# Kernel optimization log

Measured on AMD Instinct MI355X. Metric: run time of the kernel, lower is better.

The kernel has to match this reference:

```python
import jax, jax.numpy as jnp
import numpy as np
import math

IN_C = 1024
OUT_C = 1024
HEADS = 16
GROUPS = 4

def grouped_linear(src, weight, bias):
    # src: [..., in_c]; weight: [g, in_c//g, out_c//g]; bias: [out_c]
    g, icg, ocg = weight.shape
    lead = src.shape[:-1]
    s = src.reshape(*lead, g, icg)
    out = jnp.einsum('...gi,gio->...go', s, weight)
    out = out.reshape(*lead, g * ocg)
    return out + bias

def restricted_softmax(src, margin=0.0):
    src_max = jnp.maximum(jnp.max(src, axis=-1, keepdims=True), 0.0)
    out = jnp.exp(src - src_max)
    return out / (jnp.sum(out, axis=-1, keepdims=True) + jnp.exp(margin - src_max))

def setup_inputs() -> dict:
    key = jax.random.key(0)
    ks = jax.random.split(key, 9)
    B, S = 2, 2048
    icg, ocg = IN_C // GROUPS, OUT_C // GROUPS
    scale = 1.0 / math.sqrt(icg)
    return {
        'query': jax.random.normal(ks[0], (B, S, IN_C), jnp.float32),
        'key': jax.random.normal(ks[1], (B, S, IN_C), jnp.float32),
        'value': jax.random.normal(ks[2], (B, S, IN_C), jnp.float32),
        'wq': jax.random.uniform(ks[3], (GROUPS, icg, ocg), jnp.float32, -scale, scale),
        'wk': jax.random.uniform(ks[4], (GROUPS, icg, ocg), jnp.float32, -scale, scale),
        'wv': jax.random.uniform(ks[5], (GROUPS, icg, ocg), jnp.float32, -scale, scale),
        'bq': jax.random.uniform(ks[6], (OUT_C,), jnp.float32, -scale, scale),
        'bk': jax.random.uniform(ks[7], (OUT_C,), jnp.float32, -scale, scale),
        'bv': jax.random.uniform(ks[8], (OUT_C,), jnp.float32, -scale, scale),
    }

def reference(query, key, value, wq, wk, wv, bq, bk, bv):
    q = grouped_linear(query, wq, bq)   # [B,S,OUT_C]
    k = grouped_linear(key, wk, bk)
    v = grouped_linear(value, wv, bv)
    B, Sq, _ = q.shape
    Sk = k.shape[-2]
    d = OUT_C // HEADS
    q = q.reshape(B, Sq, HEADS, d).transpose(0, 2, 1, 3)  # [B,H,Sq,d]
    k = k.reshape(B, Sk, HEADS, d).transpose(0, 2, 1, 3)
    v = v.reshape(B, Sk, HEADS, d).transpose(0, 2, 1, 3)
    score = jnp.einsum('bhqd,bhkd->bhqk', q, k) / math.sqrt(d)
    attn = restricted_softmax(score)
    out = jnp.einsum('bhqk,bhkd->bhqd', attn, v)
    out = out.transpose(0, 2, 1, 3).reshape(B, Sq, OUT_C)
    return out
```

## Files before the change

kernel.cpp:

```cpp
#include <hip/hip_runtime.h>
#include <hip/hip_bf16.h>

#define BB 2
#define SS 2048
#define CC 1024
#define HH 16
#define DDIM 64
#define NROWS (BB*SS)

#define QSC 0.18033688011112042f

typedef __attribute__((ext_vector_type(8))) short bf16x8;
typedef __attribute__((ext_vector_type(4))) float f32x4;

__device__ __forceinline__ f32x4 mfma16(bf16x8 a, bf16x8 b, f32x4 c) {
    return __builtin_amdgcn_mfma_f32_16x16x32_bf16(a, b, c, 0, 0, 0);
}

__global__ __launch_bounds__(256) void prep_wt(
    const float* __restrict__ wq, const float* __restrict__ wk,
    const float* __restrict__ wv, __hip_bfloat16* __restrict__ wt)
{
    const float* w = blockIdx.z == 0 ? wq : blockIdx.z == 1 ? wk : wv;
    const int g   = blockIdx.y;
    const int kt  = blockIdx.x >> 2;
    const int ntb = blockIdx.x & 3;
    __shared__ __hip_bfloat16 Ls[64][72];
    const int t = threadIdx.x;
    #pragma unroll
    for (int j = 0; j < 4; ++j) {
        int f4 = t + j*256;
        int row = f4 >> 4, n0 = (f4 & 15) * 4;
        float4 f = *(const float4*)&w[(size_t)g*65536 + (size_t)(kt*64+row)*256
                                      + ntb*64 + n0];
        Ls[n0+0][row] = __float2bfloat16(f.x);
        Ls[n0+1][row] = __float2bfloat16(f.y);
        Ls[n0+2][row] = __float2bfloat16(f.z);
        Ls[n0+3][row] = __float2bfloat16(f.w);
    }
    __syncthreads();
    const int zg = blockIdx.z*4 + g;
    const int ch = ntb >> 1;
    #pragma unroll
    for (int j = 0; j < 2; ++j) {
        int u    = t + j*256;
        int n16g = u >> 7;
        int kss  = (u >> 6) & 1;
        int lane = u & 63;
        int l16  = lane & 15, quad = lane >> 4;
        int nt   = (ntb & 1)*4 + n16g;
        size_t frag = (((size_t)(zg*2 + ch)*4 + kt)*2 + kss)*8 + nt;
        *(uint4*)&wt[frag*512 + lane*8] =
            *(const uint4*)&Ls[n16g*16 + l16][kss*32 + quad*8];
    }
}

__global__ __launch_bounds__(256, 2) void proj_mfma(
    const float* __restrict__ qin, const float* __restrict__ kin,
    const float* __restrict__ vin,
    const __hip_bfloat16* __restrict__ wt,
    const float* __restrict__ bq, const float* __restrict__ bk,
    const float* __restrict__ bv,
    __hip_bfloat16* __restrict__ qs, __hip_bfloat16* __restrict__ ks_,
    __hip_bfloat16* __restrict__ vs)
{
    const int z = blockIdx.z;
    const float* src; const float* bias;
    if (z == 0)      { src = qin; bias = bq; }
    else if (z == 1) { src = kin; bias = bk; }
    else             { src = vin; bias = bv; }

    const int hp   = blockIdx.y;
    const int g    = hp >> 1;
    const int ch   = hp & 1;
    const int col0 = ch * 128;
    const int row0 = blockIdx.x * 128;
    const int b    = row0 >> 11;
    const int s0   = row0 & 2047;

    __shared__ char smem[36864];

    const int t    = threadIdx.x;
    const int wid  = t >> 6;
    const int lane = t & 63;
    const int l16  = lane & 15;
    const int quad = lane >> 4;

    f32x4 acc[2][8];
    #pragma unroll
    for (int mt = 0; mt < 2; ++mt)
        #pragma unroll
        for (int nt = 0; nt < 8; ++nt) acc[mt][nt] = (f32x4){0.f,0.f,0.f,0.f};

    const __hip_bfloat16* wfb = wt + ((size_t)((z*4 + g)*2 + ch) << 15);
    const float* arow0 = src + (size_t)(row0 + wid*32 +      l16)*CC + g*256;
    const float* arow1 = src + (size_t)(row0 + wid*32 + 16 + l16)*CC + g*256;

    for (int kt = 0; kt < 4; ++kt) {
        #pragma unroll
        for (int kss = 0; kss < 2; ++kss) {
            const int c0 = kt*64 + kss*32 + quad*8;
            bf16x8 af[2];
            #pragma unroll
            for (int mt = 0; mt < 2; ++mt) {
                const float* p = (mt == 0 ? arow0 : arow1) + c0;
                float4 f0 = *(const float4*)p;
                float4 f1 = *(const float4*)(p + 4);
                union { __hip_bfloat16 hh[8]; bf16x8 v; } pk;
                pk.hh[0] = __float2bfloat16(f0.x);
                pk.hh[1] = __float2bfloat16(f0.y);
                pk.hh[2] = __float2bfloat16(f0.z);
                pk.hh[3] = __float2bfloat16(f0.w);
                pk.hh[4] = __float2bfloat16(f1.x);
                pk.hh[5] = __float2bfloat16(f1.y);
                pk.hh[6] = __float2bfloat16(f1.z);
                pk.hh[7] = __float2bfloat16(f1.w);
                af[mt] = pk.v;
            }
            bf16x8 wf[8];
            #pragma unroll
            for (int nt = 0; nt < 8; ++nt)
                wf[nt] = *(const bf16x8*)
                    (wfb + (((size_t)(kt*2 + kss)*8 + nt) << 9) + lane*8);
            #pragma unroll
            for (int mt = 0; mt < 2; ++mt)
                #pragma unroll
                for (int nt = 0; nt < 8; ++nt)
                    acc[mt][nt] = mfma16(af[mt], wf[nt], acc[mt][nt]);
        }
    }

    float bval[8];
    #pragma unroll
    for (int nt = 0; nt < 8; ++nt) bval[nt] = bias[g*256 + col0 + nt*16 + l16];

    if (z < 2) {
        const float scale = (z == 0) ? QSC : 1.0f;
        auto Ot = (__hip_bfloat16 (*)[136])smem;
        #pragma unroll
        for (int mt = 0; mt < 2; ++mt)
            #pragma unroll
            for (int nt = 0; nt < 8; ++nt)
                #pragma unroll
                for (int r = 0; r < 4; ++r)
                    Ot[wid*32 + mt*16 + quad*4 + r][nt*16 + l16] =
                        __float2bfloat16((acc[mt][nt][r] + bval[nt]) * scale);
        __syncthreads();
        __hip_bfloat16* base = (z == 0) ? qs : ks_;
        #pragma unroll
        for (int j = 0; j < 8; ++j) {
            int f = wid + j*4;
            int hl = f >> 4, t16l = (f >> 1) & 7, kcs = f & 1;
            uint4 v = *(const uint4*)&Ot[t16l*16 + l16][hl*64 + kcs*32 + quad*8];
            int h = hp*2 + hl;
            int t16g = (s0 >> 4) + t16l;
            *(uint4*)&base[((size_t)(b*HH + h) << 17)
                           + ((size_t)(t16g*2 + kcs) << 9) + lane*8] = v;
        }
    } else {
        auto Vl = (__hip_bfloat16 (*)[136])smem;
        #pragma unroll
        for (int mt = 0; mt < 2; ++mt)
            #pragma unroll
            for (int nt = 0; nt < 8; ++nt) {
                union { __hip_bfloat16 hh[4]; uint2 u; } pk;
                #pragma unroll
                for (int r = 0; r < 4; ++r)
                    pk.hh[r] = __float2bfloat16(acc[mt][nt][r] + bval[nt]);
                *(uint2*)&Vl[nt*16 + l16][wid*32 + mt*16 + quad*4] = pk.u;
            }
        __syncthreads();
        const int kc0 = s0 >> 5;
        #pragma unroll
        for (int j = 0; j < 8; ++j) {
            int f = wid + j*4;
            int hl = f >> 4, dt = (f >> 2) & 3, kcl = f & 3;
            uint4 v = *(const uint4*)&Vl[hl*64 + dt*16 + l16][kcl*32 + quad*8];
            int h = hp*2 + hl;
            *(uint4*)&vs[((size_t)(b*HH + h) << 17)
                         + ((size_t)(dt*64 + kc0 + kcl) << 9) + lane*8] = v;
        }
    }
}

__global__ __launch_bounds__(256, 2) void attn_mfma(
    const __hip_bfloat16* __restrict__ qs, const __hip_bfloat16* __restrict__ ks_,
    const __hip_bfloat16* __restrict__ vs, float* __restrict__ out)
{
    const int d   = blockIdx.x;
    const int xcd = d & 7;
    const int s   = d >> 3;
    const int qt  = s & 31;
    const int bh  = (s >> 5) * 8 + xcd;
    const int h   = bh & 15;
    const int b   = bh >> 4;

    __shared__ char smem[37376];
    auto Ps = (__hip_bfloat16 (*)[64][72])smem;
    auto Ub = (float (*)[64][68])smem;
    float* Lb = (float*)(smem + 36864);

    const int t    = threadIdx.x;
    const int wid  = t >> 6;
    const int lane = t & 63;
    const int l16  = lane & 15;
    const int quad = lane >> 4;

    const __hip_bfloat16* qb = qs  + ((size_t)bh << 17);
    const __hip_bfloat16* kb = ks_ + ((size_t)bh << 17);
    const __hip_bfloat16* vb = vs  + ((size_t)bh << 17);

    const bf16x8 onesv = (bf16x8){16256,16256,16256,16256,
                                  16256,16256,16256,16256};

    bf16x8 qf[4][2];
    #pragma unroll
    for (int mt = 0; mt < 4; ++mt)
        #pragma unroll
        for (int kss = 0; kss < 2; ++kss)
            qf[mt][kss] = *(const bf16x8*)(qb +
                ((size_t)((qt*4 + mt)*2 + kss) << 9) + lane*8);

    f32x4 O[4][4];
    f32x4 Lfrag[4];
    #pragma unroll
    for (int mt = 0; mt < 4; ++mt) {
        Lfrag[mt] = (f32x4){0.f,0.f,0.f,0.f};
        #pragma unroll
        for (int dt = 0; dt < 4; ++dt) O[mt][dt] = (f32x4){0.f,0.f,0.f,0.f};
    }

    bf16x8 kf[4][2];
    #pragma unroll
    for (int nt = 0; nt < 4; ++nt)
        #pragma unroll
        for (int kss = 0; kss < 2; ++kss)
            kf[nt][kss] = *(const bf16x8*)(kb +
                ((size_t)((wid*32 + nt)*2 + kss) << 9) + lane*8);

    for (int kt = 0; kt < 8; ++kt) {
        bf16x8 vf[4][2];
        #pragma unroll
        for (int dt = 0; dt < 4; ++dt)
            #pragma unroll
            for (int kss = 0; kss < 2; ++kss)
                vf[dt][kss] = *(const bf16x8*)(vb +
                    ((size_t)(dt*64 + wid*16 + kt*2 + kss) << 9) + lane*8);

        #pragma unroll
        for (int nt = 0; nt < 4; ++nt) {
            f32x4 st[4];
            #pragma unroll
            for (int mt = 0; mt < 4; ++mt) {
                f32x4 z = (f32x4){0.f,0.f,0.f,0.f};
                z = mfma16(kf[nt][0], qf[mt][0], z);
                st[mt] = mfma16(kf[nt][1], qf[mt][1], z);
            }
            #pragma unroll
            for (int mt = 0; mt < 4; ++mt) {
                float2 e0, e1;
                e0.x = __builtin_amdgcn_exp2f(st[mt][0]);
                e0.y = __builtin_amdgcn_exp2f(st[mt][1]);
                e1.x = __builtin_amdgcn_exp2f(st[mt][2]);
                e1.y = __builtin_amdgcn_exp2f(st[mt][3]);
                union { __hip_bfloat162 h2[2]; uint2 u; } pk;
                pk.h2[0] = __float22bfloat162_rn(e0);
                pk.h2[1] = __float22bfloat162_rn(e1);
                *(uint2*)&Ps[wid][mt*16 + l16][nt*16 + quad*4] = pk.u;
            }
        }

        if (kt + 1 < 8) {
            #pragma unroll
            for (int nt = 0; nt < 4; ++nt)
                #pragma unroll
                for (int kss = 0; kss < 2; ++kss)
                    kf[nt][kss] = *(const bf16x8*)(kb +
                        ((size_t)((wid*32 + (kt+1)*4 + nt)*2 + kss) << 9) + lane*8);
        }

        #pragma unroll
        for (int kss = 0; kss < 2; ++kss) {
            bf16x8 pf[4];
            #pragma unroll
            for (int mt = 0; mt < 4; ++mt)
                pf[mt] = *(const bf16x8*)&Ps[wid][mt*16 + l16][kss*32 + quad*8];
            #pragma unroll
            for (int mt = 0; mt < 4; ++mt) {
                Lfrag[mt] = mfma16(onesv, pf[mt], Lfrag[mt]);
                #pragma unroll
                for (int dt = 0; dt < 4; ++dt)
                    O[mt][dt] = mfma16(vf[dt][kss], pf[mt], O[mt][dt]);
            }
        }
    }

    __syncthreads();
    if (wid & 1) {
        const int half = wid >> 1;
        #pragma unroll
        for (int mt = 0; mt < 4; ++mt) {
            if (quad == 0) Lb[half*64 + mt*16 + l16] = Lfrag[mt][0];
            #pragma unroll
            for (int dt = 0; dt < 4; ++dt) {
                float4 u4;
                u4.x = O[mt][dt][0]; u4.y = O[mt][dt][1];
                u4.z = O[mt][dt][2]; u4.w = O[mt][dt][3];
                *(float4*)&Ub[half][mt*16 + l16][dt*16 + quad*4] = u4;
            }
        }
    }
    __syncthreads();
    if (!(wid & 1)) {
        const int half = wid >> 1;
        #pragma unroll
        for (int mt = 0; mt < 4; ++mt) {
            Lfrag[mt][0] += Lb[half*64 + mt*16 + l16];
            #pragma unroll
            for (int dt = 0; dt < 4; ++dt) {
                float4 u4 = *(const float4*)&Ub[half][mt*16 + l16][dt*16 + quad*4];
                O[mt][dt][0] += u4.x; O[mt][dt][1] += u4.y;
                O[mt][dt][2] += u4.z; O[mt][dt][3] += u4.w;
            }
        }
    }
    if (wid == 2) {
        #pragma unroll
        for (int mt = 0; mt < 4; ++mt) {
            if (quad == 0) Lb[64 + mt*16 + l16] = Lfrag[mt][0];
            #pragma unroll
            for (int dt = 0; dt < 4; ++dt) {
                float4 u4;
                u4.x = O[mt][dt][0]; u4.y = O[mt][dt][1];
                u4.z = O[mt][dt][2]; u4.w = O[mt][dt][3];
                *(float4*)&Ub[1][mt*16 + l16][dt*16 + quad*4] = u4;
            }
        }
    }
    __syncthreads();
    if (wid == 0) {
        #pragma unroll
        for (int mt = 0; mt < 4; ++mt) {
            const float inv = 1.0f /
                (1.0f + Lfrag[mt][0] + Lb[64 + mt*16 + l16]);
            const size_t row = (size_t)b*SS + qt*64 + mt*16 + l16;
            #pragma unroll
            for (int dt = 0; dt < 4; ++dt) {
                float4 u4 = *(const float4*)&Ub[1][mt*16 + l16][dt*16 + quad*4];
                float4 o4;
                o4.x = (O[mt][dt][0] + u4.x) * inv;
                o4.y = (O[mt][dt][1] + u4.y) * inv;
                o4.z = (O[mt][dt][2] + u4.z) * inv;
                o4.w = (O[mt][dt][3] + u4.w) * inv;
                *(float4*)&out[row*CC + h*DDIM + dt*16 + quad*4] = o4;
            }
        }
    }
}

extern "C" void kernel_launch(void* const* d_in, const int* in_sizes, int n_in,
                              void* d_out, int out_size, void* d_ws, size_t ws_size,
                              hipStream_t stream) {
    (void)in_sizes; (void)n_in; (void)out_size; (void)ws_size;
    const float* qin = (const float*)d_in[0];
    const float* kin = (const float*)d_in[1];
    const float* vin = (const float*)d_in[2];
    const float* wq  = (const float*)d_in[3];
    const float* wk  = (const float*)d_in[4];
    const float* wv  = (const float*)d_in[5];
    const float* bq  = (const float*)d_in[6];
    const float* bk  = (const float*)d_in[7];
    const float* bv  = (const float*)d_in[8];

    char* w0 = (char*)d_ws;
    __hip_bfloat16* qs = (__hip_bfloat16*)(w0);
    __hip_bfloat16* ks = (__hip_bfloat16*)(w0 + 8388608);
    __hip_bfloat16* vs = (__hip_bfloat16*)(w0 + 16777216);
    __hip_bfloat16* wt = (__hip_bfloat16*)(w0 + 25165824);
    float* out = (float*)d_out;

    prep_wt<<<dim3(16, 4, 3), 256, 0, stream>>>(wq, wk, wv, wt);
    proj_mfma<<<dim3(32, 8, 3), 256, 0, stream>>>(
        qin, kin, vin, wt, bq, bk, bv, qs, ks, vs);
    attn_mfma<<<dim3(1024, 1, 1), 256, 0, stream>>>(qs, ks, vs, out);
}
```

Before: 163.2 us.

## Fuse weight bf16 conversion into projection kernel via shared-memory staging

```diff
diff --git a/kernel.cpp b/kernel.cpp
--- a/kernel.cpp
+++ b/kernel.cpp
@@ -17,58 +17,21 @@
     return __builtin_amdgcn_mfma_f32_16x16x32_bf16(a, b, c, 0, 0, 0);
 }
 
-__global__ __launch_bounds__(256) void prep_wt(
-    const float* __restrict__ wq, const float* __restrict__ wk,
-    const float* __restrict__ wv, __hip_bfloat16* __restrict__ wt)
-{
-    const float* w = blockIdx.z == 0 ? wq : blockIdx.z == 1 ? wk : wv;
-    const int g   = blockIdx.y;
-    const int kt  = blockIdx.x >> 2;
-    const int ntb = blockIdx.x & 3;
-    __shared__ __hip_bfloat16 Ls[64][72];
-    const int t = threadIdx.x;
-    #pragma unroll
-    for (int j = 0; j < 4; ++j) {
-        int f4 = t + j*256;
-        int row = f4 >> 4, n0 = (f4 & 15) * 4;
-        float4 f = *(const float4*)&w[(size_t)g*65536 + (size_t)(kt*64+row)*256
-                                      + ntb*64 + n0];
-        Ls[n0+0][row] = __float2bfloat16(f.x);
-        Ls[n0+1][row] = __float2bfloat16(f.y);
-        Ls[n0+2][row] = __float2bfloat16(f.z);
-        Ls[n0+3][row] = __float2bfloat16(f.w);
-    }
-    __syncthreads();
-    const int zg = blockIdx.z*4 + g;
-    const int ch = ntb >> 1;
-    #pragma unroll
-    for (int j = 0; j < 2; ++j) {
-        int u    = t + j*256;
-        int n16g = u >> 7;
-        int kss  = (u >> 6) & 1;
-        int lane = u & 63;
-        int l16  = lane & 15, quad = lane >> 4;
-        int nt   = (ntb & 1)*4 + n16g;
-        size_t frag = (((size_t)(zg*2 + ch)*4 + kt)*2 + kss)*8 + nt;
-        *(uint4*)&wt[frag*512 + lane*8] =
-            *(const uint4*)&Ls[n16g*16 + l16][kss*32 + quad*8];
-    }
-}
-
 __global__ __launch_bounds__(256, 2) void proj_mfma(
     const float* __restrict__ qin, const float* __restrict__ kin,
     const float* __restrict__ vin,
-    const __hip_bfloat16* __restrict__ wt,
+    const float* __restrict__ wq, const float* __restrict__ wk,
+    const float* __restrict__ wv,
     const float* __restrict__ bq, const float* __restrict__ bk,
     const float* __restrict__ bv,
     __hip_bfloat16* __restrict__ qs, __hip_bfloat16* __restrict__ ks_,
     __hip_bfloat16* __restrict__ vs)
 {
     const int z = blockIdx.z;
-    const float* src; const float* bias;
-    if (z == 0)      { src = qin; bias = bq; }
-    else if (z == 1) { src = kin; bias = bk; }
-    else             { src = vin; bias = bv; }
+    const float* src; const float* bias; const float* wsrc;
+    if (z == 0)      { src = qin; bias = bq; wsrc = wq; }
+    else if (z == 1) { src = kin; bias = bk; wsrc = wk; }
+    else             { src = vin; bias = bv; wsrc = wv; }
 
     const int hp   = blockIdx.y;
     const int g    = hp >> 1;
@@ -79,6 +42,7 @@
     const int s0   = row0 & 2047;
 
     __shared__ char smem[36864];
+    auto Ws = (__hip_bfloat16 (*)[72])smem;
 
     const int t    = threadIdx.x;
     const int wid  = t >> 6;
@@ -92,11 +56,23 @@
         #pragma unroll
         for (int nt = 0; nt < 8; ++nt) acc[mt][nt] = (f32x4){0.f,0.f,0.f,0.f};
 
-    const __hip_bfloat16* wfb = wt + ((size_t)((z*4 + g)*2 + ch) << 15);
+    const float* wg = wsrc + (size_t)g*65536;
     const float* arow0 = src + (size_t)(row0 + wid*32 +      l16)*CC + g*256;
     const float* arow1 = src + (size_t)(row0 + wid*32 + 16 + l16)*CC + g*256;
 
     for (int kt = 0; kt < 4; ++kt) {
+        #pragma unroll
+        for (int j = 0; j < 8; ++j) {
+            int idx = t + j*256;
+            int row = idx >> 5;
+            int n0  = (idx & 31) * 4;
+            float4 f = *(const float4*)&wg[(size_t)(kt*64 + row)*256 + col0 + n0];
+            Ws[n0+0][row] = __float2bfloat16(f.x);
+            Ws[n0+1][row] = __float2bfloat16(f.y);
+            Ws[n0+2][row] = __float2bfloat16(f.z);
+            Ws[n0+3][row] = __float2bfloat16(f.w);
+        }
+        __syncthreads();
         #pragma unroll
         for (int kss = 0; kss < 2; ++kss) {
             const int c0 = kt*64 + kss*32 + quad*8;
@@ -120,14 +96,14 @@
             bf16x8 wf[8];
             #pragma unroll
             for (int nt = 0; nt < 8; ++nt)
-                wf[nt] = *(const bf16x8*)
-                    (wfb + (((size_t)(kt*2 + kss)*8 + nt) << 9) + lane*8);
+                wf[nt] = *(const bf16x8*)&Ws[nt*16 + l16][kss*32 + quad*8];
             #pragma unroll
             for (int mt = 0; mt < 2; ++mt)
                 #pragma unroll
                 for (int nt = 0; nt < 8; ++nt)
                     acc[mt][nt] = mfma16(af[mt], wf[nt], acc[mt][nt]);
         }
+        __syncthreads();
     }
 
     float bval[8];
@@ -376,11 +352,9 @@
     __hip_bfloat16* qs = (__hip_bfloat16*)(w0);
     __hip_bfloat16* ks = (__hip_bfloat16*)(w0 + 8388608);
     __hip_bfloat16* vs = (__hip_bfloat16*)(w0 + 16777216);
-    __hip_bfloat16* wt = (__hip_bfloat16*)(w0 + 25165824);
     float* out = (float*)d_out;
 
-    prep_wt<<<dim3(16, 4, 3), 256, 0, stream>>>(wq, wk, wv, wt);
     proj_mfma<<<dim3(32, 8, 3), 256, 0, stream>>>(
-        qin, kin, vin, wt, bq, bk, bv, qs, ks, vs);
+        qin, kin, vin, wq, wk, wv, bq, bk, bv, qs, ks, vs);
     attn_mfma<<<dim3(1024, 1, 1), 256, 0, stream>>>(qs, ks, vs, out);
 }
```

After: 171.4 us. 1.05x slower.
